# Kernel tuning notes

Measured on AMD Instinct MI355X. Metric: run time of the kernel, lower is better.

Reference implementation:

```python
import jax, jax.numpy as jnp
import numpy as np
from jax.scipy.linalg import expm as _expm

B, D = 1024, 128
_SQRT3 = 3.0 ** 0.5
_C1, _C2 = 0.5 - _SQRT3 / 6.0, 0.5 + _SQRT3 / 6.0


def setup_inputs() -> dict:
    key = jax.random.key(0)
    k_t, k_y, k_a, k_w = jax.random.split(key, 4)
    scale = 1.0 / np.sqrt(D)  # keep ||Omega|| moderate so expm is well-conditioned
    return {
        "t0": jax.random.uniform(k_t, (B,), dtype=jnp.float32),
        "h": jnp.float32(0.1),
        "y0": jax.random.normal(k_y, (B, D), dtype=jnp.float32),
        "A0": jax.random.normal(k_a, (B, D, D), dtype=jnp.float32) * scale,
        "W": jax.random.normal(k_w, (B, D, D), dtype=jnp.float32) * scale,
    }


def reference(t0, h, y0, A0, W):
    # A(t) = A0 + t * W evaluated at the two Gauss-Legendre nodes
    t1 = t0 + _C1 * h  # (B,)
    t2 = t0 + _C2 * h  # (B,)
    A1 = A0 + t1[:, None, None] * W  # (B, D, D)
    A2 = A0 + t2[:, None, None] * W  # (B, D, D)
    alpha1 = (h * 0.5) * (A1 + A2)
    alpha2 = (h * _SQRT3) * (A2 - A1)
    comm = alpha1 @ alpha2 - alpha2 @ alpha1  # [alpha1, alpha2]
    Omega = alpha1 - comm / 12.0
    U = jax.vmap(_expm)(Omega)  # batched matrix exponential (B, D, D)
    y_next = jnp.einsum("bij,bj->bi", U, y0)  # (B, D)
    return y_next, jnp.stack((A1, A2), axis=0)
```

## Files before the change

### kernel.cpp

```cpp
#include <hip/hip_runtime.h>

#define B_SZ 1024
#define D_SZ 128
#define KTERMS 8

__device__ inline float dot_regs(const float* r, const float* v) {
    float a0 = 0.f, a1 = 0.f, a2 = 0.f, a3 = 0.f;
#pragma unroll
    for (int j = 0; j < D_SZ; j += 8) {
        float4 v0 = *(const float4*)(v + j);
        float4 v1 = *(const float4*)(v + j + 4);
        a0 = fmaf(r[j + 0], v0.x, a0);
        a1 = fmaf(r[j + 1], v0.y, a1);
        a2 = fmaf(r[j + 2], v0.z, a2);
        a3 = fmaf(r[j + 3], v0.w, a3);
        a0 = fmaf(r[j + 4], v1.x, a0);
        a1 = fmaf(r[j + 5], v1.y, a1);
        a2 = fmaf(r[j + 6], v1.z, a2);
        a3 = fmaf(r[j + 7], v1.w, a3);
    }
    return (a0 + a1) + (a2 + a3);
}

__global__ void __launch_bounds__(256, 2)
magnus_kernel(const float* __restrict__ t0p, const float* __restrict__ hp,
              const float* __restrict__ y0, const float* __restrict__ A0,
              const float* __restrict__ W, float* __restrict__ out)
{
    __shared__ __align__(16) float sv[D_SZ];
    __shared__ __align__(16) float su1[D_SZ];
    __shared__ __align__(16) float su2[D_SZ];
    __shared__ __align__(16) float su3[D_SZ];
    __shared__ __align__(16) float su4[D_SZ];

    const int b = blockIdx.x;
    const int tid = threadIdx.x;
    const float h = hp[0];
    const float tb = t0p[b];
    const float SQ3_6 = 0.28867513459481287f;
    const float t1 = tb + (0.5f - SQ3_6) * h;
    const float t2 = tb + (0.5f + SQ3_6) * h;

    const size_t moff = (size_t)b * (D_SZ * D_SZ);
    const float4* A0v = (const float4*)(A0 + moff);
    const float4* Wv  = (const float4*)(W + moff);
    float4* o1 = (float4*)(out + (size_t)B_SZ * D_SZ + moff);
    float4* o2 = (float4*)(out + (size_t)B_SZ * D_SZ
                               + (size_t)B_SZ * D_SZ * D_SZ + moff);

#pragma unroll 4
    for (int it = 0; it < 16; ++it) {
        int i = it * 256 + tid;
        float4 a = A0v[i];
        float4 w = Wv[i];
        float4 p1, p2;
        p1.x = fmaf(t1, w.x, a.x);
        p1.y = fmaf(t1, w.y, a.y);
        p1.z = fmaf(t1, w.z, a.z);
        p1.w = fmaf(t1, w.w, a.w);
        p2.x = fmaf(t2, w.x, a.x);
        p2.y = fmaf(t2, w.y, a.y);
        p2.z = fmaf(t2, w.z, a.z);
        p2.w = fmaf(t2, w.w, a.w);
        o1[i] = p1;
        o2[i] = p2;
    }

    float r[D_SZ];
    {
        const float4* src = (tid < D_SZ)
            ? (const float4*)(A0 + moff + (size_t)tid * D_SZ)
            : (const float4*)(W + moff + (size_t)(tid - D_SZ) * D_SZ);
#pragma unroll
        for (int j = 0; j < D_SZ / 4; ++j) {
            float4 q = src[j];
            r[4 * j + 0] = q.x;
            r[4 * j + 1] = q.y;
            r[4 * j + 2] = q.z;
            r[4 * j + 3] = q.w;
        }
    }

    float yacc = 0.0f;
    if (tid < D_SZ) {
        float v = y0[(size_t)b * D_SZ + tid];
        sv[tid] = v;
        yacc = v;
    }
    __syncthreads();

    const float hs = h * (tb + 0.5f * h);
    const float c3 = h * h * h * (1.0f / 12.0f);

    for (int k = 1; k <= KTERMS; ++k) {
        float accA = dot_regs(r, sv);
        if (tid < D_SZ) su1[tid] = accA; else su2[tid - D_SZ] = accA;
        __syncthreads();
        const float* vb = (tid < D_SZ) ? su2 : su1;
        float accB = dot_regs(r, vb);
        if (tid < D_SZ) su3[tid] = accB; else su4[tid - D_SZ] = accB;
        __syncthreads();
        if (tid < D_SZ) {
            float wn = h * su1[tid] + hs * su2[tid] - c3 * (su3[tid] - su4[tid]);
            wn *= (1.0f / (float)k);
            yacc += wn;
            sv[tid] = wn;
        }
        __syncthreads();
    }

    if (tid < D_SZ) {
        out[(size_t)b * D_SZ + tid] = yacc;
    }
}

extern "C" void kernel_launch(void* const* d_in, const int* in_sizes, int n_in,
                              void* d_out, int out_size, void* d_ws, size_t ws_size,
                              hipStream_t stream) {
    const float* t0 = (const float*)d_in[0];
    const float* h  = (const float*)d_in[1];
    const float* y0 = (const float*)d_in[2];
    const float* A0 = (const float*)d_in[3];
    const float* W  = (const float*)d_in[4];
    float* out = (float*)d_out;
    magnus_kernel<<<B_SZ, 256, 0, stream>>>(t0, h, y0, A0, W, out);
}
```

Before: 267.0 us.

## Split matrix rows across thread pairs with 512-thread blocks and nontemporal stores

Doubles the block to 512 threads so that each thread holds half a matrix row (64 registers instead of 128). Partial dot products are combined with a lane shuffle. This cuts register pressure and raises occupancy and per-block parallelism for the Taylor-series matvec loop. The stores of A1/A2 now use nontemporal writes to avoid polluting the cache, and the extra shuffle adds a small cost per step.

```diff
diff --git a/kernel.cpp b/kernel.cpp
--- a/kernel.cpp
+++ b/kernel.cpp
@@ -4,10 +4,12 @@
 #define D_SZ 128
 #define KTERMS 8
 
-__device__ inline float dot_regs(const float* r, const float* v) {
+typedef float vfloat4 __attribute__((ext_vector_type(4)));
+
+__device__ inline float dot64(const float* r, const float* v) {
     float a0 = 0.f, a1 = 0.f, a2 = 0.f, a3 = 0.f;
 #pragma unroll
-    for (int j = 0; j < D_SZ; j += 8) {
+    for (int j = 0; j < 64; j += 8) {
         float4 v0 = *(const float4*)(v + j);
         float4 v1 = *(const float4*)(v + j + 4);
         a0 = fmaf(r[j + 0], v0.x, a0);
@@ -22,7 +24,7 @@
     return (a0 + a1) + (a2 + a3);
 }
 
-__global__ void __launch_bounds__(256, 2)
+__global__ void __launch_bounds__(512, 4)
 magnus_kernel(const float* __restrict__ t0p, const float* __restrict__ hp,
               const float* __restrict__ y0, const float* __restrict__ A0,
               const float* __restrict__ W, float* __restrict__ out)
@@ -44,16 +46,16 @@
     const size_t moff = (size_t)b * (D_SZ * D_SZ);
     const float4* A0v = (const float4*)(A0 + moff);
     const float4* Wv  = (const float4*)(W + moff);
-    float4* o1 = (float4*)(out + (size_t)B_SZ * D_SZ + moff);
-    float4* o2 = (float4*)(out + (size_t)B_SZ * D_SZ
-                               + (size_t)B_SZ * D_SZ * D_SZ + moff);
+    vfloat4* o1 = (vfloat4*)(out + (size_t)B_SZ * D_SZ + moff);
+    vfloat4* o2 = (vfloat4*)(out + (size_t)B_SZ * D_SZ
+                                 + (size_t)B_SZ * D_SZ * D_SZ + moff);
 
 #pragma unroll 4
-    for (int it = 0; it < 16; ++it) {
-        int i = it * 256 + tid;
+    for (int it = 0; it < 8; ++it) {
+        int i = it * 512 + tid;
         float4 a = A0v[i];
         float4 w = Wv[i];
-        float4 p1, p2;
+        vfloat4 p1, p2;
         p1.x = fmaf(t1, w.x, a.x);
         p1.y = fmaf(t1, w.y, a.y);
         p1.z = fmaf(t1, w.z, a.z);
@@ -62,23 +64,22 @@
         p2.y = fmaf(t2, w.y, a.y);
         p2.z = fmaf(t2, w.z, a.z);
         p2.w = fmaf(t2, w.w, a.w);
-        o1[i] = p1;
-        o2[i] = p2;
+        __builtin_nontemporal_store(p1, o1 + i);
+        __builtin_nontemporal_store(p2, o2 + i);
     }
 
-    float r[D_SZ];
-    {
-        const float4* src = (tid < D_SZ)
-            ? (const float4*)(A0 + moff + (size_t)tid * D_SZ)
-            : (const float4*)(W + moff + (size_t)(tid - D_SZ) * D_SZ);
+    const int half = tid & 1;
+    const int row  = (tid >> 1) & 127;
+    const float* rbase = (tid < 256) ? (A0 + moff) : (W + moff);
+    const float4* src = (const float4*)(rbase + (size_t)row * D_SZ + half * 64);
+    float r[64];
 #pragma unroll
-        for (int j = 0; j < D_SZ / 4; ++j) {
-            float4 q = src[j];
-            r[4 * j + 0] = q.x;
-            r[4 * j + 1] = q.y;
-            r[4 * j + 2] = q.z;
-            r[4 * j + 3] = q.w;
-        }
+    for (int j = 0; j < 16; ++j) {
+        float4 q = src[j];
+        r[4 * j + 0] = q.x;
+        r[4 * j + 1] = q.y;
+        r[4 * j + 2] = q.z;
+        r[4 * j + 3] = q.w;
     }
 
     float yacc = 0.0f;
@@ -93,12 +94,14 @@
     const float c3 = h * h * h * (1.0f / 12.0f);
 
     for (int k = 1; k <= KTERMS; ++k) {
-        float accA = dot_regs(r, sv);
-        if (tid < D_SZ) su1[tid] = accA; else su2[tid - D_SZ] = accA;
+        float a = dot64(r, sv + half * 64);
+        a += __shfl_xor(a, 1);
+        if (tid < 256) su1[row] = a; else su2[row] = a;
         __syncthreads();
-        const float* vb = (tid < D_SZ) ? su2 : su1;
-        float accB = dot_regs(r, vb);
-        if (tid < D_SZ) su3[tid] = accB; else su4[tid - D_SZ] = accB;
+        const float* vb = (tid < 256) ? su2 : su1;
+        float c = dot64(r, vb + half * 64);
+        c += __shfl_xor(c, 1);
+        if (tid < 256) su3[row] = c; else su4[row] = c;
         __syncthreads();
         if (tid < D_SZ) {
             float wn = h * su1[tid] + hs * su2[tid] - c3 * (su3[tid] - su4[tid]);
@@ -123,5 +126,5 @@
     const float* A0 = (const float*)d_in[3];
     const float* W  = (const float*)d_in[4];
     float* out = (float*)d_out;
-    magnus_kernel<<<B_SZ, 256, 0, stream>>>(t0, h, y0, A0, W, out);
+    magnus_kernel<<<B_SZ, 512, 0, stream>>>(t0, h, y0, A0, W, out);
 }
```

Result: faster. 258.8 us (-3.1%).
